# Kernel optimization log

Hardware: AMD Instinct MI355X
Metric: run time of the kernel (lower is better)

## Reference

```python
import jax, jax.numpy as jnp
import numpy as np

TEMPERATURE = 0.07

def _l2norm(x):
    return x / jnp.linalg.norm(x, axis=-1, keepdims=True)

def setup_inputs() -> dict:
    key = jax.random.key(0)
    k1, k2, k3, k4 = jax.random.split(key, 4)
    B, T, C_ctx, C_enc, P, K = 8, 256, 512, 256, 12, 128
    context = jax.random.normal(k1, (B, T, C_ctx), dtype=jnp.float32)
    encoded = jax.random.normal(k2, (B, T, C_enc), dtype=jnp.float32)
    W = jax.random.normal(k3, (P, C_enc, C_ctx), dtype=jnp.float32) * (1.0 / np.sqrt(C_ctx))
    neg_idx = jax.random.randint(k4, (P, B * (T - 1), K), 0, B * T, dtype=jnp.int64)
    return {"context": context, "encoded": encoded, "W": W, "neg_idx": neg_idx}

def reference(context, encoded, W, neg_idx):
    B, T, C_enc = encoded.shape
    n_pred = W.shape[0]
    # normalized pool of all encoded vectors [B*T, C_enc]
    pool = _l2norm(encoded.reshape(B * T, C_enc))
    total = jnp.float32(0.0)
    for k in range(1, n_pred + 1):  # fixed small loop over horizons
        Nk = B * (T - k)
        c_t = context[:, : T - k, :]                       # [B, T-k, C_ctx]
        z_hat = jnp.einsum('btc,ec->bte', c_t, W[k - 1])   # [B, T-k, C_enc]
        z_hat = _l2norm(z_hat.reshape(Nk, C_enc))
        z_pos = _l2norm(encoded[:, k:, :].reshape(Nk, C_enc))
        pos_logits = jnp.sum(z_hat * z_pos, axis=-1, keepdims=True)  # [Nk, 1]
        z_neg = pool[neg_idx[k - 1, :Nk]]                  # [Nk, K, C_enc]
        neg_logits = jnp.einsum('nc,nkc->nk', z_hat, z_neg)
        logits = jnp.concatenate([pos_logits, neg_logits], axis=1) / TEMPERATURE
        # cross-entropy with target class 0
        step_loss = jnp.mean(jax.nn.logsumexp(logits, axis=-1) - logits[:, 0])
        total = total + step_loss
    return total / n_pred
```

## Files before the change

kernel.cpp:

```cpp
#include <hip/hip_runtime.h>
#include <hip/hip_bf16.h>

typedef __attribute__((ext_vector_type(8))) short short8;
typedef __attribute__((ext_vector_type(4))) float f32x4;
typedef _Float16 __attribute__((ext_vector_type(2))) half2v;

#define INV_TEMP 14.285714285714286f
#define LOGIT_MAX 14.2857143f
#define L2E 1.44269504f
#define OFFE (LOGIT_MAX * L2E)
#define PCLIP 0.23f
#define PDELTA (PCLIP / 7.f)
#define PQS (7.f / PCLIP)

__device__ __forceinline__ ushort bf16c(float f) {
  uint u = __float_as_uint(f);
  uint r = (u + 0x7fffu + ((u >> 16) & 1u)) >> 16;
  return (ushort)r;
}
__device__ __forceinline__ uint pk2(float a, float b) {
  return (uint)bf16c(a) | ((uint)bf16c(b) << 16);
}
__device__ __forceinline__ uint pkh(float a, float b) {
  return __builtin_bit_cast(uint, __builtin_amdgcn_cvt_pkrtz(a, b));
}
__device__ __forceinline__ half2v h2(uint u) {
  return __builtin_bit_cast(half2v, u);
}
__device__ __forceinline__ int sdot4_(uint a, uint b, int c) {
  return __builtin_amdgcn_sdot4((int)a, (int)b, c, false);
}

template <int CTRL>
__device__ __forceinline__ float dpp_add(float v) {
  const int x = __builtin_amdgcn_mov_dpp(__float_as_int(v), CTRL, 0xF, 0xF, true);
  return v + __int_as_float(x);
}
template <int CTRL>
__device__ __forceinline__ int dpp_addi(int v) {
  return v + __builtin_amdgcn_mov_dpp(v, CTRL, 0xF, 0xF, true);
}
__device__ __forceinline__ float qsum16(float v) {
  v = dpp_add<0xB1>(v);
  v = dpp_add<0x4E>(v);
  v = dpp_add<0x141>(v);
  v = dpp_add<0x140>(v);
  return v;
}
__device__ __forceinline__ int qsum8i(int v) {
  v = dpp_addi<0xB1>(v);
  v = dpp_addi<0x4E>(v);
  v = dpp_addi<0x141>(v);
  return v;
}

__global__ __launch_bounds__(256) void cvt_bf16_kernel(
    const float* __restrict__ ctx, const float* __restrict__ W,
    ushort* __restrict__ ctxb, ushort* __restrict__ Wb) {
  const int bid = blockIdx.x;
  const float* in;
  ushort* out;
  size_t i;
  if (bid < 512) { in = ctx; out = ctxb; i = (size_t)bid * 256 + threadIdx.x; }
  else           { in = W;   out = Wb;   i = (size_t)(bid - 512) * 256 + threadIdx.x; }
  const float4 a = *(const float4*)(in + i * 8);
  const float4 b = *(const float4*)(in + i * 8 + 4);
  const uint4 o = make_uint4(pk2(a.x, a.y), pk2(a.z, a.w), pk2(b.x, b.y), pk2(b.z, b.w));
  *(uint4*)(out + i * 8) = o;
}

__global__ __launch_bounds__(256) void pool_norm_kernel(
    const float* __restrict__ enc, uint* __restrict__ pool4,
    float* __restrict__ acc) {
  const int tid = threadIdx.x;
  if (blockIdx.x == 0 && tid < 12) acc[tid] = 0.f;
  const int grp = tid >> 4, lane = tid & 15;
  const int r = blockIdx.x * 16 + grp;
  const float* src = enc + (size_t)r * 256 + lane * 16;
  float4 v0 = *(const float4*)(src);
  float4 v1 = *(const float4*)(src + 4);
  float4 v2 = *(const float4*)(src + 8);
  float4 v3 = *(const float4*)(src + 12);
  float c[16] = {v0.x, v0.y, v0.z, v0.w, v1.x, v1.y, v1.z, v1.w,
                 v2.x, v2.y, v2.z, v2.w, v3.x, v3.y, v3.z, v3.w};
  float ss = 0.f;
#pragma unroll
  for (int i = 0; i < 16; ++i) ss = fmaf(c[i], c[i], ss);
  ss = qsum16(ss);
  const float qs = rsqrtf(ss) * PQS;
  uint w0 = 0, w1 = 0;
#pragma unroll
  for (int n = 0; n < 8; ++n) {
    const int q0 = (int)rintf(fminf(fmaxf(c[n] * qs, -7.f), 7.f)) + 8;
    const int q1 = (int)rintf(fminf(fmaxf(c[8 + n] * qs, -7.f), 7.f)) + 8;
    w0 |= (uint)q0 << (4 * n);
    w1 |= (uint)q1 << (4 * n);
  }
  *(uint2*)(pool4 + (size_t)r * 32 + lane * 2) = make_uint2(w0, w1);
}

__global__ __launch_bounds__(256) void zhat_gemm_kernel(
    const ushort* __restrict__ ctxb, const ushort* __restrict__ Wb,
    uint* __restrict__ Zp) {
  const int kk = blockIdx.z;
  const int Tk = 255 - kk, Nk = 8 * Tk;
  const int rowbase = blockIdx.y * 64;
  if (rowbase >= Nk) return;
  const int colbase = blockIdx.x * 128;

  __shared__ ushort As[64 * 40];
  __shared__ ushort Bs[128 * 40];

  const int tid = threadIdx.x;
  const int arow = tid & 63;
  const int akseg = (tid >> 6) * 8;
  int n = rowbase + arow;
  if (n >= Nk) n = Nk - 1;
  const int bb = n / Tk, tt = n - bb * Tk;
  const ushort* aptr = ctxb + ((size_t)(bb * 256 + tt)) * 512 + akseg;
  const int brow = tid & 127;
  const int bk0 = (tid >> 7) * 8;
  const ushort* bptr = Wb + ((size_t)kk * 256 + colbase + brow) * 512 + bk0;

  const int wid = tid >> 6, lane = tid & 63;
  const int wm = wid >> 1, wn = wid & 1;
  const int l15 = lane & 15, l16 = lane >> 4;

  f32x4 acc[2][4];
#pragma unroll
  for (int i = 0; i < 2; ++i)
#pragma unroll
    for (int j = 0; j < 4; ++j) acc[i][j] = (f32x4){0.f, 0.f, 0.f, 0.f};

  const ushort* aread = &As[(wm * 32 + l15) * 40 + l16 * 8];
  const ushort* bread = &Bs[(wn * 64 + l15) * 40 + l16 * 8];

  for (int k0 = 0; k0 < 512; k0 += 32) {
    const uint4 av = *(const uint4*)(aptr + k0);
    const uint4 bv0 = *(const uint4*)(bptr + k0);
    const uint4 bv1 = *(const uint4*)(bptr + k0 + 16);
    __syncthreads();
    *(uint4*)&As[arow * 40 + akseg] = av;
    *(uint4*)&Bs[brow * 40 + bk0] = bv0;
    *(uint4*)&Bs[brow * 40 + bk0 + 16] = bv1;
    __syncthreads();
    short8 bf[4];
#pragma unroll
    for (int nb = 0; nb < 4; ++nb) bf[nb] = *(const short8*)(bread + nb * 16 * 40);
#pragma unroll
    for (int mb = 0; mb < 2; ++mb) {
      short8 af = *(const short8*)(aread + mb * 16 * 40);
#pragma unroll
      for (int nb = 0; nb < 4; ++nb)
        acc[mb][nb] = __builtin_amdgcn_mfma_f32_16x16x32_bf16(af, bf[nb], acc[mb][nb], 0, 0, 0);
    }
  }

#pragma unroll
  for (int mb = 0; mb < 2; ++mb) {
    const int row0 = rowbase + wm * 32 + mb * 16 + l16 * 4;
#pragma unroll
    for (int r = 0; r < 4; ++r) {
      const int row = row0 + r;
      if (row < Nk) {
        uint* zp = Zp + ((size_t)kk * 2040 + row) * 128 + (colbase >> 1) + wn * 32 + l15;
        zp[0]  = pkh(acc[mb][0][r], acc[mb][1][r]);
        zp[16] = pkh(acc[mb][2][r], acc[mb][3][r]);
      }
    }
  }
}

#define DOTN(P) ({                                                              \
    int d0_ = 0, d1_ = 0;                                                       \
    uint e_, o_;                                                                \
    e_ = P.x & 0x0F0F0F0Fu; o_ = (P.x >> 4) & 0x0F0F0F0Fu;                      \
    d0_ = sdot4_(zq[0], e_, d0_); d1_ = sdot4_(zq[4], o_, d1_);                 \
    e_ = P.y & 0x0F0F0F0Fu; o_ = (P.y >> 4) & 0x0F0F0F0Fu;                      \
    d0_ = sdot4_(zq[1], e_, d0_); d1_ = sdot4_(zq[5], o_, d1_);                 \
    e_ = P.z & 0x0F0F0F0Fu; o_ = (P.z >> 4) & 0x0F0F0F0Fu;                      \
    d0_ = sdot4_(zq[2], e_, d0_); d1_ = sdot4_(zq[6], o_, d1_);                 \
    e_ = P.w & 0x0F0F0F0Fu; o_ = (P.w >> 4) & 0x0F0F0F0Fu;                      \
    d0_ = sdot4_(zq[3], e_, d0_); d1_ = sdot4_(zq[7], o_, d1_);                 \
    qsum8i(d0_ + d1_); })

#define LDB(P, IDX) P = *(const uint4*)(pbase + (size_t)(uint)(IDX) * 32);
#define ACCB(SUM, P) SUM += exp2f(fmaf((float)DOTN(P), kG, c2m));

__global__ __launch_bounds__(256) void loss_kernel(
    const uint* __restrict__ Zp, const uint* __restrict__ pool4,
    const int* __restrict__ neg_idx, float* __restrict__ acc) {
  const int kk = blockIdx.y;
  const int Tk = 255 - kk, Nk = 8 * Tk;
  if ((int)(blockIdx.x * 16) >= Nk) return;
  const int tid = threadIdx.x;
  const int n = blockIdx.x * 16 + (tid >> 4);
  const int l = tid & 15;
  const int h = l >> 3;
  const int g = l & 7;
  float row_loss = 0.f;
  if (n < Nk) {
    const uint* zr = Zp + ((size_t)kk * 2040 + n) * 128 + g * 16;
    uint zu[16];
#pragma unroll
    for (int i = 0; i < 4; ++i) *(uint4*)(zu + 4 * i) = *(const uint4*)(zr + 4 * i);
    float zf[32];
#pragma unroll
    for (int c = 0; c < 16; ++c) {
      const half2v hv = h2(zu[c]);
      zf[c] = (float)hv.x;
      zf[16 + c] = (float)hv.y;
    }
    float ss = 0.f;
#pragma unroll
    for (int i = 0; i < 32; ++i) ss = fmaf(zf[i], zf[i], ss);
    ss = dpp_add<0xB1>(ss); ss = dpp_add<0x4E>(ss); ss = dpp_add<0x141>(ss);
    const float s127 = rsqrtf(ss) * 127.f;
    uint zq[8];
#pragma unroll
    for (int t = 0; t < 4; ++t) {
      const uint e0 = (uint)((int)rintf(zf[8 * t]     * s127) & 255);
      const uint e1 = (uint)((int)rintf(zf[8 * t + 2] * s127) & 255);
      const uint e2 = (uint)((int)rintf(zf[8 * t + 4] * s127) & 255);
      const uint e3 = (uint)((int)rintf(zf[8 * t + 6] * s127) & 255);
      zq[t] = e0 | (e1 << 8) | (e2 << 16) | (e3 << 24);
      const uint o0 = (uint)((int)rintf(zf[8 * t + 1] * s127) & 255);
      const uint o1 = (uint)((int)rintf(zf[8 * t + 3] * s127) & 255);
      const uint o2 = (uint)((int)rintf(zf[8 * t + 5] * s127) & 255);
      const uint o3 = (uint)((int)rintf(zf[8 * t + 7] * s127) & 255);
      zq[t + 4] = o0 | (o1 << 8) | (o2 << 16) | (o3 << 24);
    }
    int nq = 0, zs = 0;
#pragma unroll
    for (int t = 0; t < 8; ++t) {
      nq = sdot4_(zq[t], zq[t], nq);
      zs = sdot4_(zq[t], 0x01010101u, zs);
    }
    nq = qsum8i(nq);
    zs = qsum8i(zs);
    const float kG = (INV_TEMP * L2E * PDELTA) * rsqrtf((float)nq);
    const float c2 = -8.f * (float)zs * kG;
    const float c2m = c2 - OFFE;

    const uint* pbase = pool4 + g * 4;
    const int bb = n / Tk, tt = n - bb * Tk;
    uint4 PP;
    LDB(PP, bb * 256 + tt + kk + 1)
    const float pose = fmaf((float)DOTN(PP), kG, c2);

    const int* ip = neg_idx + ((size_t)kk * 2040 + n) * 128 + h * 64;
    float s0 = 0.f, s1 = 0.f, s2 = 0.f, s3 = 0.f;
    uint4 A, B, C, D, E, F, G, H;
    {
      const int4 iv = *(const int4*)ip;
      LDB(A, iv.x) LDB(B, iv.y) LDB(C, iv.z) LDB(D, iv.w)
    }
    for (int j8 = 0; j8 < 8; ++j8) {
      {
        const int4 jv = *(const int4*)(ip + j8 * 8 + 4);
        LDB(E, jv.x) LDB(F, jv.y) LDB(G, jv.z) LDB(H, jv.w)
      }
      ACCB(s0, A) ACCB(s1, B) ACCB(s2, C) ACCB(s3, D)
      if (j8 < 7) {
        const int4 kv = *(const int4*)(ip + j8 * 8 + 8);
        LDB(A, kv.x) LDB(B, kv.y) LDB(C, kv.z) LDB(D, kv.w)
      }
      ACCB(s0, E) ACCB(s1, F) ACCB(s2, G) ACCB(s3, H)
    }
    float sl = (s0 + s1) + (s2 + s3);
    sl = dpp_add<0x140>(sl);
    const float ssum = sl + exp2f(pose - OFFE);
    row_loss = LOGIT_MAX + 0.69314718f * (__log2f(ssum) - pose);
  }
  __shared__ float bl[16];
  if (l == 0) bl[tid >> 4] = row_loss;
  __syncthreads();
  if (tid == 0) {
    float s = 0.f;
#pragma unroll
    for (int i = 0; i < 16; ++i) s += bl[i];
    atomicAdd(&acc[kk], s);
  }
}

__global__ void finalize_kernel(const float* __restrict__ acc,
                                float* __restrict__ out) {
  if (threadIdx.x == 0) {
    float tot = 0.f;
#pragma unroll
    for (int kk = 0; kk < 12; ++kk) tot += acc[kk] / (8.0f * (255 - kk));
    out[0] = tot / 12.0f;
  }
}

extern "C" void kernel_launch(void* const* d_in, const int* in_sizes, int n_in,
                              void* d_out, int out_size, void* d_ws, size_t ws_size,
                              hipStream_t stream) {
  const float* ctx = (const float*)d_in[0];
  const float* enc = (const float*)d_in[1];
  const float* W   = (const float*)d_in[2];
  const int*   neg = (const int*)d_in[3];
  float* out = (float*)d_out;

  char* ws = (char*)d_ws;
  uint*   pool4 = (uint*)(ws);
  ushort* ctxb  = (ushort*)(ws + 262144);
  ushort* Wb    = (ushort*)(ws + 2359296);
  uint*   Zp    = (uint*)(ws + 5505024);
  float*  accb  = (float*)(ws + 18038784);

  cvt_bf16_kernel<<<dim3(1280), dim3(256), 0, stream>>>(ctx, W, ctxb, Wb);
  pool_norm_kernel<<<dim3(128), dim3(256), 0, stream>>>(enc, pool4, accb);
  zhat_gemm_kernel<<<dim3(2, 32, 12), dim3(256), 0, stream>>>(ctxb, Wb, Zp);
  loss_kernel<<<dim3(128, 12), dim3(256), 0, stream>>>(Zp, pool4, neg, accb);
  finalize_kernel<<<dim3(1), dim3(64), 0, stream>>>(accb, out);
}
```

Measured before the change: 69.19 us.

## Merge prep kernels and stage GEMM tiles via direct global-to-LDS loads

Fuses the bf16 conversion and pool normalization kernels into one launch, removing one kernel launch and its gap. Rewrites the z_hat GEMM tile staging to use global_load_lds so data goes from global memory straight into shared memory without passing through registers. This requires reorganizing the LDS layout into k-segment-major blocks of 8 elements. The new layout drops the row padding, which may bring back LDS bank conflicts on the MFMA fragment reads.

```diff
diff --git a/kernel.cpp b/kernel.cpp
--- a/kernel.cpp
+++ b/kernel.cpp
@@ -30,6 +30,11 @@
 __device__ __forceinline__ int sdot4_(uint a, uint b, int c) {
   return __builtin_amdgcn_sdot4((int)a, (int)b, c, false);
 }
+__device__ __forceinline__ void gl_lds16(const void* g, void* l) {
+  __builtin_amdgcn_global_load_lds(
+      (const __attribute__((address_space(1))) void*)g,
+      (__attribute__((address_space(3))) void*)l, 16, 0, 0);
+}
 
 template <int CTRL>
 __device__ __forceinline__ float dpp_add(float v) {
@@ -54,28 +59,28 @@
   return v;
 }
 
-__global__ __launch_bounds__(256) void cvt_bf16_kernel(
+__global__ __launch_bounds__(256) void prep_kernel(
     const float* __restrict__ ctx, const float* __restrict__ W,
-    ushort* __restrict__ ctxb, ushort* __restrict__ Wb) {
+    const float* __restrict__ enc, ushort* __restrict__ ctxb,
+    ushort* __restrict__ Wb, uint* __restrict__ pool4,
+    float* __restrict__ acc) {
   const int bid = blockIdx.x;
-  const float* in;
-  ushort* out;
-  size_t i;
-  if (bid < 512) { in = ctx; out = ctxb; i = (size_t)bid * 256 + threadIdx.x; }
-  else           { in = W;   out = Wb;   i = (size_t)(bid - 512) * 256 + threadIdx.x; }
-  const float4 a = *(const float4*)(in + i * 8);
-  const float4 b = *(const float4*)(in + i * 8 + 4);
-  const uint4 o = make_uint4(pk2(a.x, a.y), pk2(a.z, a.w), pk2(b.x, b.y), pk2(b.z, b.w));
-  *(uint4*)(out + i * 8) = o;
-}
-
-__global__ __launch_bounds__(256) void pool_norm_kernel(
-    const float* __restrict__ enc, uint* __restrict__ pool4,
-    float* __restrict__ acc) {
   const int tid = threadIdx.x;
-  if (blockIdx.x == 0 && tid < 12) acc[tid] = 0.f;
+  if (bid < 1280) {
+    const float* in;
+    ushort* out;
+    size_t i;
+    if (bid < 512) { in = ctx; out = ctxb; i = (size_t)bid * 256 + tid; }
+    else           { in = W;   out = Wb;   i = (size_t)(bid - 512) * 256 + tid; }
+    const float4 a = *(const float4*)(in + i * 8);
+    const float4 b = *(const float4*)(in + i * 8 + 4);
+    const uint4 o = make_uint4(pk2(a.x, a.y), pk2(a.z, a.w), pk2(b.x, b.y), pk2(b.z, b.w));
+    *(uint4*)(out + i * 8) = o;
+    return;
+  }
+  if (bid == 1280 && tid < 12) acc[tid] = 0.f;
   const int grp = tid >> 4, lane = tid & 15;
-  const int r = blockIdx.x * 16 + grp;
+  const int r = (bid - 1280) * 16 + grp;
   const float* src = enc + (size_t)r * 256 + lane * 16;
   float4 v0 = *(const float4*)(src);
   float4 v1 = *(const float4*)(src + 4);
@@ -108,10 +113,11 @@
   if (rowbase >= Nk) return;
   const int colbase = blockIdx.x * 128;
 
-  __shared__ ushort As[64 * 40];
-  __shared__ ushort Bs[128 * 40];
+  __shared__ __attribute__((aligned(16))) ushort As[64 * 32];
+  __shared__ __attribute__((aligned(16))) ushort Bs[128 * 32];
 
   const int tid = threadIdx.x;
+  const int wid = tid >> 6, lane = tid & 63;
   const int arow = tid & 63;
   const int akseg = (tid >> 6) * 8;
   int n = rowbase + arow;
@@ -119,10 +125,12 @@
   const int bb = n / Tk, tt = n - bb * Tk;
   const ushort* aptr = ctxb + ((size_t)(bb * 256 + tt)) * 512 + akseg;
   const int brow = tid & 127;
-  const int bk0 = (tid >> 7) * 8;
-  const ushort* bptr = Wb + ((size_t)kk * 256 + colbase + brow) * 512 + bk0;
-
-  const int wid = tid >> 6, lane = tid & 63;
+  const int bke = (tid >> 7) * 8;
+  const ushort* bptr = Wb + ((size_t)kk * 256 + colbase + brow) * 512 + bke;
+
+  char* As_w = (char*)As + wid * 1024;
+  char* Bs_w = (char*)Bs + wid * 1024;
+
   const int wm = wid >> 1, wn = wid & 1;
   const int l15 = lane & 15, l16 = lane >> 4;
 
@@ -132,24 +140,21 @@
 #pragma unroll
     for (int j = 0; j < 4; ++j) acc[i][j] = (f32x4){0.f, 0.f, 0.f, 0.f};
 
-  const ushort* aread = &As[(wm * 32 + l15) * 40 + l16 * 8];
-  const ushort* bread = &Bs[(wn * 64 + l15) * 40 + l16 * 8];
+  const ushort* aread = As + (size_t)(l16 * 64 + wm * 32 + l15) * 8;
+  const ushort* bread = Bs + (size_t)(l16 * 128 + wn * 64 + l15) * 8;
 
   for (int k0 = 0; k0 < 512; k0 += 32) {
-    const uint4 av = *(const uint4*)(aptr + k0);
-    const uint4 bv0 = *(const uint4*)(bptr + k0);
-    const uint4 bv1 = *(const uint4*)(bptr + k0 + 16);
     __syncthreads();
-    *(uint4*)&As[arow * 40 + akseg] = av;
-    *(uint4*)&Bs[brow * 40 + bk0] = bv0;
-    *(uint4*)&Bs[brow * 40 + bk0 + 16] = bv1;
+    gl_lds16(aptr + k0, As_w);
+    gl_lds16(bptr + k0, Bs_w);
+    gl_lds16(bptr + k0 + 16, Bs_w + 4096);
     __syncthreads();
     short8 bf[4];
 #pragma unroll
-    for (int nb = 0; nb < 4; ++nb) bf[nb] = *(const short8*)(bread + nb * 16 * 40);
+    for (int nb = 0; nb < 4; ++nb) bf[nb] = *(const short8*)(bread + (size_t)nb * 16 * 8);
 #pragma unroll
     for (int mb = 0; mb < 2; ++mb) {
-      short8 af = *(const short8*)(aread + mb * 16 * 40);
+      short8 af = *(const short8*)(aread + (size_t)mb * 16 * 8);
 #pragma unroll
       for (int nb = 0; nb < 4; ++nb)
         acc[mb][nb] = __builtin_amdgcn_mfma_f32_16x16x32_bf16(af, bf[nb], acc[mb][nb], 0, 0, 0);
@@ -309,8 +314,7 @@
   uint*   Zp    = (uint*)(ws + 5505024);
   float*  accb  = (float*)(ws + 18038784);
 
-  cvt_bf16_kernel<<<dim3(1280), dim3(256), 0, stream>>>(ctx, W, ctxb, Wb);
-  pool_norm_kernel<<<dim3(128), dim3(256), 0, stream>>>(enc, pool4, accb);
+  prep_kernel<<<dim3(1408), dim3(256), 0, stream>>>(ctx, W, enc, ctxb, Wb, pool4, accb);
   zhat_gemm_kernel<<<dim3(2, 32, 12), dim3(256), 0, stream>>>(ctxb, Wb, Zp);
   loss_kernel<<<dim3(128, 12), dim3(256), 0, stream>>>(Zp, pool4, neg, accb);
   finalize_kernel<<<dim3(1), dim3(64), 0, stream>>>(accb, out);
```

Result: faster. 66.36 us (-4.1%).
